# Kernel tuning notes

Measured on AMD Instinct MI355X. Metric: run time of the kernel, lower is better.

Reference implementation:

```python
import jax, jax.numpy as jnp
import numpy as np

EPS = 1e-6
NUM_HEADS = 16

def layer_norm(x, w, b):
    mu = jnp.mean(x, axis=-1, keepdims=True)
    var = jnp.mean(jnp.square(x - mu), axis=-1, keepdims=True)
    return (x - mu) * jax.lax.rsqrt(var + EPS) * w + b

def setup_inputs() -> dict:
    key = jax.random.key(0)
    ks = jax.random.split(key, 8)
    B, N, C = 32, 577, 1024
    H = 4 * C
    s = lambda d: 1.0 / np.sqrt(d)
    return {
        "x": jax.random.normal(ks[0], (B, N, C), jnp.float32),
        "ln1_w": jnp.ones((C,), jnp.float32),
        "ln1_b": jnp.zeros((C,), jnp.float32),
        "qkv_w": jax.random.normal(ks[1], (3 * C, C), jnp.float32) * s(C),
        "qkv_b": jnp.zeros((3 * C,), jnp.float32),
        "proj_w": jax.random.normal(ks[2], (C, C), jnp.float32) * s(C),
        "proj_b": jnp.zeros((C,), jnp.float32),
        "ln2_w": jnp.ones((C,), jnp.float32),
        "ln2_b": jnp.zeros((C,), jnp.float32),
        "fc1_w": jax.random.normal(ks[3], (H, C), jnp.float32) * s(C),
        "fc1_b": jnp.zeros((H,), jnp.float32),
        "fc2_w": jax.random.normal(ks[4], (C, H), jnp.float32) * s(H),
        "fc2_b": jnp.zeros((C,), jnp.float32),
    }

def reference(x, ln1_w, ln1_b, qkv_w, qkv_b, proj_w, proj_b,
              ln2_w, ln2_b, fc1_w, fc1_b, fc2_w, fc2_b):
    B, N, C = x.shape
    Hh = NUM_HEADS
    Dh = C // Hh
    scale = Dh ** -0.5

    # --- attention branch ---
    h = layer_norm(x, ln1_w, ln1_b)
    qkv = h @ qkv_w.T + qkv_b                      # [B,N,3C]
    qkv = qkv.reshape(B, N, 3, Hh, Dh).transpose(2, 0, 3, 1, 4)  # [3,B,H,N,Dh]
    q, k, v = qkv[0] * scale, qkv[1], qkv[2]
    attn = jnp.einsum("bhqd,bhkd->bhqk", q, k)     # [B,H,N,N]
    attn = jax.nn.softmax(attn, axis=-1)
    o = jnp.einsum("bhqk,bhkd->bhqd", attn, v)     # [B,H,N,Dh]
    o = o.transpose(0, 2, 1, 3).reshape(B, N, C)
    x = x + (o @ proj_w.T + proj_b)

    # --- MLP branch ---
    h = layer_norm(x, ln2_w, ln2_b)
    h = jax.nn.gelu(h @ fc1_w.T + fc1_b, approximate=False)
    x = x + (h @ fc2_w.T + fc2_b)
    return x
```

## Files before the change

kernel.cpp:

```cpp
#include <hip/hip_runtime.h>
#include <math.h>

#define BATCH  32
#define NTOK   577
#define CDIM   1024
#define C3DIM  3072
#define H4DIM  4096
#define NHEAD  16
#define MROWS  (BATCH * NTOK)
#define NPADV  584

typedef __bf16 bf16x8 __attribute__((ext_vector_type(8)));
typedef float  f32x4  __attribute__((ext_vector_type(4)));
typedef unsigned short u16x8 __attribute__((ext_vector_type(8)));

__device__ __forceinline__ float bf2f(unsigned short u) {
    union { unsigned int i; float f; } v; v.i = ((unsigned int)u) << 16; return v.f;
}
__device__ __forceinline__ unsigned short f2bf(float f) {
    union { float f; unsigned int i; } v; v.f = f;
    unsigned int r = v.i + 0x7FFFu + ((v.i >> 16) & 1u);
    return (unsigned short)(r >> 16);
}
__device__ __forceinline__ bf16x8 ld_bf8(const unsigned short* p) {
    return __builtin_bit_cast(bf16x8, *(const u16x8*)p);
}

typedef const __attribute__((address_space(1))) unsigned int* gptr_t;
typedef __attribute__((address_space(3))) unsigned int* lptr_t;
__device__ __forceinline__ void gl2lds(const void* g, const void* l) {
    __builtin_amdgcn_global_load_lds(
        (gptr_t)(unsigned long long)g,
        (lptr_t)(unsigned int)(unsigned long long)l,
        16, 0, 0);
}

#define QSCALE 0.18033688011112042f

__global__ __launch_bounds__(256) void conv_kernel(const float* __restrict__ src,
                                                   unsigned short* __restrict__ dst, int n) {
    int i = (blockIdx.x * 256 + threadIdx.x) * 4;
    if (i < n) {
        float4 v = *(const float4*)(src + i);
        dst[i]     = f2bf(v.x);
        dst[i + 1] = f2bf(v.y);
        dst[i + 2] = f2bf(v.z);
        dst[i + 3] = f2bf(v.w);
    }
}

template<bool F32IN>
__global__ __launch_bounds__(256) void ln_kernel(
    const void* __restrict__ X,
    const float* __restrict__ w,
    const float* __restrict__ b,
    unsigned short* __restrict__ out)
{
    const int row = blockIdx.x;
    const int t = threadIdx.x;
    float vals[4]; float s = 0.f, ss = 0.f;
#pragma unroll
    for (int i = 0; i < 4; i++) {
        int c = t + i * 256;
        float v;
        if (F32IN) v = ((const float*)X)[(size_t)row * CDIM + c];
        else       v = bf2f(((const unsigned short*)X)[(size_t)row * CDIM + c]);
        vals[i] = v; s += v; ss += v * v;
    }
#pragma unroll
    for (int off = 32; off > 0; off >>= 1) { s += __shfl_xor(s, off); ss += __shfl_xor(ss, off); }
    __shared__ float red[8];
    if ((t & 63) == 0) { red[t >> 6] = s; red[4 + (t >> 6)] = ss; }
    __syncthreads();
    s  = red[0] + red[1] + red[2] + red[3];
    ss = red[4] + red[5] + red[6] + red[7];
    float mu  = s * (1.f / CDIM);
    float var = ss * (1.f / CDIM) - mu * mu;
    float rs  = rsqrtf(var + 1e-6f);
#pragma unroll
    for (int i = 0; i < 4; i++) {
        int c = t + i * 256;
        float o = (vals[i] - mu) * rs * w[c] + b[c];
        out[(size_t)row * CDIM + c] = f2bf(o);
    }
}

template<int OP>
__global__ __launch_bounds__(512, 2) void gemm256(
    const unsigned short* __restrict__ A,
    const unsigned short* __restrict__ W, int Wstride,
    const unsigned short* __restrict__ bias,
    const void* __restrict__ Res,
    void* __restrict__ Out,
    void* __restrict__ Out2,
    void* __restrict__ Out3,
    int K, int Nout)
{
    __shared__ __align__(16) unsigned short Alds[2][256 * 64];
    __shared__ __align__(16) unsigned short Blds[2][256 * 64];

    const int tid  = threadIdx.x;
    const int lane = tid & 63, wave = tid >> 6;
    const int q = lane >> 4, l16 = lane & 15;
    const int wm = (wave >> 2) << 7;
    const int wn = (wave & 3) << 6;
    const int tileM = blockIdx.y << 8, tileN = blockIdx.x << 8;

    f32x4 acc[8][4];
#pragma unroll
    for (int i = 0; i < 8; i++)
#pragma unroll
        for (int j = 0; j < 4; j++) acc[i][j] = (f32x4){0.f, 0.f, 0.f, 0.f};

    const int srow = tid >> 3;
    const int scol = (tid & 7) << 3;
    const unsigned short* pA[4];
    const unsigned short* pB[4];
#pragma unroll
    for (int j = 0; j < 4; j++) {
        int ra = tileM + j * 64 + srow; if (ra > MROWS - 1) ra = MROWS - 1;
        pA[j] = A + (size_t)ra * K + scol;
        pB[j] = W + (size_t)(tileN + j * 64 + srow) * Wstride + scol;
    }

    auto STAGE = [&](int buf, int k0) {
#pragma unroll
        for (int j = 0; j < 4; j++) {
            gl2lds(pA[j] + k0, &Alds[buf][j * 4096 + wave * 512]);
            gl2lds(pB[j] + k0, &Blds[buf][j * 4096 + wave * 512]);
        }
    };

    auto COMPUTE = [&](int buf) {
#pragma unroll
        for (int ks = 0; ks < 2; ks++) {
            bf16x8 af[8], bfr[4];
#pragma unroll
            for (int mi = 0; mi < 8; mi++)
                af[mi] = ld_bf8(&Alds[buf][(wm + mi * 16 + l16) * 64 + ks * 32 + q * 8]);
#pragma unroll
            for (int ni = 0; ni < 4; ni++)
                bfr[ni] = ld_bf8(&Blds[buf][(wn + ni * 16 + l16) * 64 + ks * 32 + q * 8]);
#pragma unroll
            for (int mi = 0; mi < 8; mi++)
#pragma unroll
                for (int ni = 0; ni < 4; ni++)
                    acc[mi][ni] = __builtin_amdgcn_mfma_f32_16x16x32_bf16(af[mi], bfr[ni], acc[mi][ni], 0, 0, 0);
        }
    };

    const int NT = K >> 6;
    STAGE(0, 0);
    __syncthreads();
    int cur = 0;
    for (int t = 0; t < NT; ++t) {
        if (t + 1 < NT) STAGE(cur ^ 1, (t + 1) << 6);
        COMPUTE(cur);
        __syncthreads();
        cur ^= 1;
    }

#pragma unroll
    for (int mi = 0; mi < 8; mi++) {
#pragma unroll
        for (int r = 0; r < 4; r++) {
            int row = tileM + wm + mi * 16 + q * 4 + r;
            if (row >= MROWS) continue;
            unsigned int bb = 0, nn = 0;
            if constexpr (OP == 0) {
                bb = ((unsigned int)row * 58154u) >> 25;
                nn = (unsigned int)row - bb * 577u;
            }
#pragma unroll
            for (int ni = 0; ni < 4; ni++) {
                int col = tileN + wn + ni * 16 + l16;
                size_t oidx = (size_t)row * Nout + col;
                float v = acc[mi][ni][r];
                if constexpr (OP != 4) v += bf2f(bias[col]);
                if constexpr (OP == 0) {
                    int s = col >> 10, h = (col >> 6) & 15, d = col & 63;
                    size_t bh = (size_t)(bb * 16 + h);
                    if (s == 0)      ((unsigned short*)Out )[(bh * NTOK + nn) * 64 + d] = f2bf(v * QSCALE);
                    else if (s == 1) ((unsigned short*)Out2)[(bh * NTOK + nn) * 64 + d] = f2bf(v);
                    else             ((unsigned short*)Out3)[(bh * 64 + d) * NPADV + nn] = f2bf(v);
                } else if constexpr (OP == 1) {
                    v += ((const float*)Res)[oidx];
                    ((unsigned short*)Out)[oidx] = f2bf(v);
                } else if constexpr (OP == 2) {
                    float z = exp2f(v * fmaf(v * v, 0.1029432f, 2.3022082f));
                    v = v - v * __builtin_amdgcn_rcpf(1.0f + z);
                    ((unsigned short*)Out)[oidx] = f2bf(v);
                } else if constexpr (OP == 3) {
                    v += bf2f(((const unsigned short*)Res)[oidx]);
                    ((float*)Out)[oidx] = v;
                } else {
                    ((float*)Out)[oidx] += v;
                }
            }
        }
    }
}

__global__ __launch_bounds__(256) void attn_kernel(
    const unsigned short* __restrict__ Qb,
    const unsigned short* __restrict__ Kb,
    const unsigned short* __restrict__ Vt,
    unsigned short* __restrict__ o)
{
    const int flat = blockIdx.x;
    const int x8 = flat & 7;
    const int g = flat >> 3;
    const int qt = g % 10;
    const int bh = (g / 10) * 8 + x8;
    const int q0 = qt * 64;
    const int tid = threadIdx.x;
    const int wv = tid >> 6, lane = tid & 63;
    const int qd = lane >> 4, l16 = lane & 15;

    __shared__ __align__(16) unsigned short Ps[4][16 * 72];

    const unsigned short* Qh = Qb + (size_t)bh * NTOK * 64;
    const unsigned short* Kh = Kb + (size_t)bh * NTOK * 64;
    const unsigned short* Vh = Vt + (size_t)bh * 64 * NPADV;

    int qrow = q0 + wv * 16 + l16;
    int qr = qrow < NTOK ? qrow : NTOK - 1;
    bf16x8 qf0 = ld_bf8(Qh + (size_t)qr * 64 + qd * 8);
    bf16x8 qf1 = ld_bf8(Qh + (size_t)qr * 64 + 32 + qd * 8);

    float lsum[4];
    f32x4 Oacc[4];
#pragma unroll
    for (int r = 0; r < 4; r++) lsum[r] = 0.f;
#pragma unroll
    for (int ni = 0; ni < 4; ni++) Oacc[ni] = (f32x4){0.f, 0.f, 0.f, 0.f};

    for (int kt = 0; kt < 10; kt++) {
        const int k0 = kt * 64;
        const bool tail = (kt == 9);
        f32x4 sacc[4];
#pragma unroll
        for (int ni = 0; ni < 4; ni++) sacc[ni] = (f32x4){0.f, 0.f, 0.f, 0.f};
#pragma unroll
        for (int ni = 0; ni < 4; ni++) {
            int krow = k0 + ni * 16 + l16;
            if (krow > NTOK - 1) krow = NTOK - 1;
            const unsigned short* kp = Kh + (size_t)krow * 64 + qd * 8;
            bf16x8 b0 = ld_bf8(kp);
            bf16x8 b1 = ld_bf8(kp + 32);
            sacc[ni] = __builtin_amdgcn_mfma_f32_16x16x32_bf16(qf0, b0, sacc[ni], 0, 0, 0);
            sacc[ni] = __builtin_amdgcn_mfma_f32_16x16x32_bf16(qf1, b1, sacc[ni], 0, 0, 0);
        }

#pragma unroll
        for (int r = 0; r < 4; r++) {
#pragma unroll
            for (int ni = 0; ni < 4; ni++) {
                float pv = exp2f(sacc[ni][r]);
                if (tail && (k0 + ni * 16 + l16 >= NTOK)) pv = 0.f;
                lsum[r] += pv;
                Ps[wv][(qd * 4 + r) * 72 + ni * 16 + l16] = f2bf(pv);
            }
        }

#pragma unroll
        for (int kk = 0; kk < 2; kk++) {
            bf16x8 a = ld_bf8(&Ps[wv][l16 * 72 + kk * 32 + qd * 8]);
            int kchunk = k0 + kk * 32 + qd * 8;
            if (kchunk > NTOK - 1) kchunk = NTOK - 1;
#pragma unroll
            for (int ni = 0; ni < 4; ni++) {
                bf16x8 bb = ld_bf8(Vh + (size_t)(ni * 16 + l16) * NPADV + kchunk);
                Oacc[ni] = __builtin_amdgcn_mfma_f32_16x16x32_bf16(a, bb, Oacc[ni], 0, 0, 0);
            }
        }
    }

#pragma unroll
    for (int r = 0; r < 4; r++)
#pragma unroll
        for (int off = 8; off > 0; off >>= 1) lsum[r] += __shfl_xor(lsum[r], off);

    const int b = bh >> 4, h = bh & 15;
#pragma unroll
    for (int r = 0; r < 4; r++) {
        int gq = q0 + wv * 16 + qd * 4 + r;
        if (gq >= NTOK) continue;
        float inv = 1.0f / lsum[r];
#pragma unroll
        for (int ni = 0; ni < 4; ni++) {
            int d = ni * 16 + l16;
            o[((size_t)b * NTOK + gq) * CDIM + (size_t)h * 64 + d] = f2bf(Oacc[ni][r] * inv);
        }
    }
}

extern "C" void kernel_launch(void* const* d_in, const int* in_sizes, int n_in,
                              void* d_out, int out_size, void* d_ws, size_t ws_size,
                              hipStream_t stream) {
    (void)in_sizes; (void)n_in; (void)out_size;
    const float* x      = (const float*)d_in[0];
    const float* ln1_w  = (const float*)d_in[1];
    const float* ln1_b  = (const float*)d_in[2];
    const float* qkv_w  = (const float*)d_in[3];
    const float* qkv_b  = (const float*)d_in[4];
    const float* proj_w = (const float*)d_in[5];
    const float* proj_b = (const float*)d_in[6];
    const float* ln2_w  = (const float*)d_in[7];
    const float* ln2_b  = (const float*)d_in[8];
    const float* fc1_w  = (const float*)d_in[9];
    const float* fc1_b  = (const float*)d_in[10];
    const float* fc2_w  = (const float*)d_in[11];
    const float* fc2_b  = (const float*)d_in[12];

    char* ws = (char*)d_ws;
    size_t off = 0;
    auto alloc = [&](size_t els) { void* p = ws + off; off += els * 2; return (unsigned short*)p; };
    unsigned short* qkvw_b  = alloc(3145728);
    unsigned short* projw_b = alloc(1048576);
    unsigned short* fc1w_b  = alloc(4194304);
    unsigned short* fc2w_b  = alloc(4194304);
    unsigned short* qkvb_b  = alloc(3072);
    unsigned short* projb_b = alloc(1024);
    unsigned short* fc1b_b  = alloc(4096);
    unsigned short* fc2b_b  = alloc(1024);
    off = (off + 255) & ~(size_t)255;
    unsigned short* R1 = (unsigned short*)(ws + off); off += (size_t)MROWS * 1024 * 2;
    unsigned short* R2 = (unsigned short*)(ws + off); off += (size_t)512 * 64 * NPADV * 2;
    unsigned short* R3 = (unsigned short*)(ws + off);
    size_t rem = ws_size > off ? ws_size - off : 0;
    const int CH = rem >= (size_t)MROWS * H4DIM * 2 ? H4DIM
                 : (rem >= (size_t)MROWS * 1024 * 2 ? 1024
                 : (rem >= (size_t)MROWS * 512 * 2 ? 512 : 256));

    unsigned short* Qb   = (unsigned short*)d_out;
    unsigned short* h1   = Qb + (size_t)MROWS * 1024;
    unsigned short* obuf = h1;
    unsigned short* Kb = R1;
    unsigned short* Vt = R2;
    unsigned short* x1 = R1;
    unsigned short* h2 = R2;

    conv_kernel<<<3145728 / 1024, 256, 0, stream>>>(qkv_w,  qkvw_b,  3145728);
    conv_kernel<<<1048576 / 1024, 256, 0, stream>>>(proj_w, projw_b, 1048576);
    conv_kernel<<<4194304 / 1024, 256, 0, stream>>>(fc1_w,  fc1w_b,  4194304);
    conv_kernel<<<4194304 / 1024, 256, 0, stream>>>(fc2_w,  fc2w_b,  4194304);
    conv_kernel<<<3, 256, 0, stream>>>(qkv_b,  qkvb_b,  3072);
    conv_kernel<<<1, 256, 0, stream>>>(proj_b, projb_b, 1024);
    conv_kernel<<<4, 256, 0, stream>>>(fc1_b,  fc1b_b,  4096);
    conv_kernel<<<1, 256, 0, stream>>>(fc2_b,  fc2b_b,  1024);

    const int mt = (MROWS + 255) / 256;

    ln_kernel<true><<<MROWS, 256, 0, stream>>>(x, ln1_w, ln1_b, h1);
    gemm256<0><<<dim3(C3DIM / 256, mt), 512, 0, stream>>>(
        h1, qkvw_b, CDIM, qkvb_b, nullptr, Qb, Kb, Vt, CDIM, C3DIM);
    attn_kernel<<<5120, 256, 0, stream>>>(Qb, Kb, Vt, obuf);
    gemm256<1><<<dim3(CDIM / 256, mt), 512, 0, stream>>>(
        obuf, projw_b, CDIM, projb_b, x, x1, nullptr, nullptr, CDIM, CDIM);
    ln_kernel<false><<<MROWS, 256, 0, stream>>>(x1, ln2_w, ln2_b, h2);

    if (CH == H4DIM) {
        gemm256<2><<<dim3(H4DIM / 256, mt), 512, 0, stream>>>(
            h2, fc1w_b, CDIM, fc1b_b, nullptr, R3, nullptr, nullptr, CDIM, H4DIM);
        gemm256<3><<<dim3(CDIM / 256, mt), 512, 0, stream>>>(
            R3, fc2w_b, H4DIM, fc2b_b, x1, d_out, nullptr, nullptr, H4DIM, CDIM);
    } else {
        for (int c0 = 0; c0 < H4DIM; c0 += CH) {
            gemm256<2><<<dim3(CH / 256, mt), 512, 0, stream>>>(
                h2, fc1w_b + (size_t)c0 * CDIM, CDIM, fc1b_b + c0, nullptr, R3, nullptr, nullptr, CDIM, CH);
            if (c0 == 0)
                gemm256<3><<<dim3(CDIM / 256, mt), 512, 0, stream>>>(
                    R3, fc2w_b, H4DIM, fc2b_b, x1, d_out, nullptr, nullptr, CH, CDIM);
            else
                gemm256<4><<<dim3(CDIM / 256, mt), 512, 0, stream>>>(
                    R3, fc2w_b + c0, H4DIM, nullptr, nullptr, d_out, nullptr, nullptr, CH, CDIM);
        }
    }
}
```

Baseline: 1.263 ms.

## Use 128x128 tile GEMM for N=1024 projection and fc2 layers

Adds a smaller 128x128-tile GEMM kernel with 256 threads and uses it for the attention projection and fc2 GEMMs, whose output width of 1024 gave few blocks with 256x256 tiles. The large-tile kernel is kept only for the QKV and fc1 GEMMs, and its epilogue is simplified accordingly. The goal is better CU occupancy and load balance on the narrow GEMMs. The cost is less data reuse and a single-buffered, sync-heavy K loop in the new kernel.

```diff
diff --git a/kernel.cpp b/kernel.cpp
--- a/kernel.cpp
+++ b/kernel.cpp
@@ -36,6 +36,11 @@
 }
 
 #define QSCALE 0.18033688011112042f
+
+__device__ __forceinline__ float gelu_f(float v) {
+    float z = exp2f(v * fmaf(v * v, 0.1029432f, 2.3022082f));
+    return v - v * __builtin_amdgcn_rcpf(1.0f + z);
+}
 
 __global__ __launch_bounds__(256) void conv_kernel(const float* __restrict__ src,
                                                    unsigned short* __restrict__ dst, int n) {
@@ -86,11 +91,87 @@
 }
 
 template<int OP>
+__global__ __launch_bounds__(256) void gemm128(
+    const unsigned short* __restrict__ A,
+    const unsigned short* __restrict__ W, int Wstride,
+    const unsigned short* __restrict__ bias,
+    const void* __restrict__ Res,
+    void* __restrict__ Out,
+    int K, int Nout)
+{
+    __shared__ __align__(16) unsigned short Alds[128 * 32];
+    __shared__ __align__(16) unsigned short Blds[128 * 32];
+    const int tid  = threadIdx.x;
+    const int lane = tid & 63, wave = tid >> 6;
+    const int q = lane >> 4, l16 = lane & 15;
+    const int wm = (wave & 1) << 6, wn = (wave >> 1) << 6;
+    const int tileM = blockIdx.y << 7, tileN = blockIdx.x << 7;
+
+    f32x4 acc[4][4];
+#pragma unroll
+    for (int i = 0; i < 4; i++)
+#pragma unroll
+        for (int j = 0; j < 4; j++) acc[i][j] = (f32x4){0.f, 0.f, 0.f, 0.f};
+
+    const int srow = tid >> 2;
+    const int soff = (tid & 3) << 3;
+    int arow1 = tileM + srow;       if (arow1 > MROWS - 1) arow1 = MROWS - 1;
+    int arow2 = tileM + srow + 64;  if (arow2 > MROWS - 1) arow2 = MROWS - 1;
+    const unsigned short* Aptr  = A + (size_t)arow1 * K + soff;
+    const unsigned short* Aptr2 = A + (size_t)arow2 * K + soff;
+    const unsigned short* Wp    = W + (size_t)(tileN + srow) * Wstride + soff;
+    const unsigned short* Wp2   = Wp + (size_t)64 * Wstride;
+
+    for (int k0 = 0; k0 < K; k0 += 32) {
+        __syncthreads();
+        gl2lds(Aptr  + k0, &Alds[wave * 512]);
+        gl2lds(Aptr2 + k0, &Alds[2048 + wave * 512]);
+        gl2lds(Wp    + k0, &Blds[wave * 512]);
+        gl2lds(Wp2   + k0, &Blds[2048 + wave * 512]);
+        __syncthreads();
+        bf16x8 af[4], bfr[4];
+#pragma unroll
+        for (int mi = 0; mi < 4; mi++) af[mi]  = ld_bf8(&Alds[(wm + mi * 16 + l16) * 32 + q * 8]);
+#pragma unroll
+        for (int ni = 0; ni < 4; ni++) bfr[ni] = ld_bf8(&Blds[(wn + ni * 16 + l16) * 32 + q * 8]);
+#pragma unroll
+        for (int mi = 0; mi < 4; mi++)
+#pragma unroll
+            for (int ni = 0; ni < 4; ni++)
+                acc[mi][ni] = __builtin_amdgcn_mfma_f32_16x16x32_bf16(af[mi], bfr[ni], acc[mi][ni], 0, 0, 0);
+    }
+
+#pragma unroll
+    for (int mi = 0; mi < 4; mi++) {
+#pragma unroll
+        for (int r = 0; r < 4; r++) {
+            int row = tileM + wm + mi * 16 + q * 4 + r;
+            if (row >= MROWS) continue;
+#pragma unroll
+            for (int ni = 0; ni < 4; ni++) {
+                int col = tileN + wn + ni * 16 + l16;
+                size_t oidx = (size_t)row * Nout + col;
+                float v = acc[mi][ni][r];
+                if constexpr (OP != 4) v += bf2f(bias[col]);
+                if constexpr (OP == 1) {
+                    v += ((const float*)Res)[oidx];
+                    ((unsigned short*)Out)[oidx] = f2bf(v);
+                } else if constexpr (OP == 3) {
+                    v += bf2f(((const unsigned short*)Res)[oidx]);
+                    ((float*)Out)[oidx] = v;
+                } else {
+                    ((float*)Out)[oidx] += v;
+                }
+            }
+        }
+    }
+}
+
+template<int OP>
 __global__ __launch_bounds__(512, 2) void gemm256(
     const unsigned short* __restrict__ A,
     const unsigned short* __restrict__ W, int Wstride,
     const unsigned short* __restrict__ bias,
-    const void* __restrict__ Res,
     void* __restrict__ Out,
     void* __restrict__ Out2,
     void* __restrict__ Out3,
@@ -175,26 +256,15 @@
             for (int ni = 0; ni < 4; ni++) {
                 int col = tileN + wn + ni * 16 + l16;
                 size_t oidx = (size_t)row * Nout + col;
-                float v = acc[mi][ni][r];
-                if constexpr (OP != 4) v += bf2f(bias[col]);
+                float v = acc[mi][ni][r] + bf2f(bias[col]);
                 if constexpr (OP == 0) {
                     int s = col >> 10, h = (col >> 6) & 15, d = col & 63;
                     size_t bh = (size_t)(bb * 16 + h);
                     if (s == 0)      ((unsigned short*)Out )[(bh * NTOK + nn) * 64 + d] = f2bf(v * QSCALE);
                     else if (s == 1) ((unsigned short*)Out2)[(bh * NTOK + nn) * 64 + d] = f2bf(v);
                     else             ((unsigned short*)Out3)[(bh * 64 + d) * NPADV + nn] = f2bf(v);
-                } else if constexpr (OP == 1) {
-                    v += ((const float*)Res)[oidx];
-                    ((unsigned short*)Out)[oidx] = f2bf(v);
-                } else if constexpr (OP == 2) {
-                    float z = exp2f(v * fmaf(v * v, 0.1029432f, 2.3022082f));
-                    v = v - v * __builtin_amdgcn_rcpf(1.0f + z);
-                    ((unsigned short*)Out)[oidx] = f2bf(v);
-                } else if constexpr (OP == 3) {
-                    v += bf2f(((const unsigned short*)Res)[oidx]);
-                    ((float*)Out)[oidx] = v;
                 } else {
-                    ((float*)Out)[oidx] += v;
+                    ((unsigned short*)Out)[oidx] = f2bf(gelu_f(v));
                 }
             }
         }
@@ -350,31 +420,32 @@
     conv_kernel<<<4, 256, 0, stream>>>(fc1_b,  fc1b_b,  4096);
     conv_kernel<<<1, 256, 0, stream>>>(fc2_b,  fc2b_b,  1024);
 
-    const int mt = (MROWS + 255) / 256;
+    const int mt128 = (MROWS + 127) / 128;
+    const int mt256 = (MROWS + 255) / 256;
 
     ln_kernel<true><<<MROWS, 256, 0, stream>>>(x, ln1_w, ln1_b, h1);
-    gemm256<0><<<dim3(C3DIM / 256, mt), 512, 0, stream>>>(
-        h1, qkvw_b, CDIM, qkvb_b, nullptr, Qb, Kb, Vt, CDIM, C3DIM);
+    gemm256<0><<<dim3(C3DIM / 256, mt256), 512, 0, stream>>>(
+        h1, qkvw_b, CDIM, qkvb_b, Qb, Kb, Vt, CDIM, C3DIM);
     attn_kernel<<<5120, 256, 0, stream>>>(Qb, Kb, Vt, obuf);
-    gemm256<1><<<dim3(CDIM / 256, mt), 512, 0, stream>>>(
-        obuf, projw_b, CDIM, projb_b, x, x1, nullptr, nullptr, CDIM, CDIM);
+    gemm128<1><<<dim3(CDIM / 128, mt128), 256, 0, stream>>>(
+        obuf, projw_b, CDIM, projb_b, x, x1, CDIM, CDIM);
     ln_kernel<false><<<MROWS, 256, 0, stream>>>(x1, ln2_w, ln2_b, h2);
 
     if (CH == H4DIM) {
-        gemm256<2><<<dim3(H4DIM / 256, mt), 512, 0, stream>>>(
-            h2, fc1w_b, CDIM, fc1b_b, nullptr, R3, nullptr, nullptr, CDIM, H4DIM);
-        gemm256<3><<<dim3(CDIM / 256, mt), 512, 0, stream>>>(
-            R3, fc2w_b, H4DIM, fc2b_b, x1, d_out, nullptr, nullptr, H4DIM, CDIM);
+        gemm256<2><<<dim3(H4DIM / 256, mt256), 512, 0, stream>>>(
+            h2, fc1w_b, CDIM, fc1b_b, R3, nullptr, nullptr, CDIM, H4DIM);
+        gemm128<3><<<dim3(CDIM / 128, mt128), 256, 0, stream>>>(
+            R3, fc2w_b, H4DIM, fc2b_b, x1, d_out, H4DIM, CDIM);
     } else {
         for (int c0 = 0; c0 < H4DIM; c0 += CH) {
-            gemm256<2><<<dim3(CH / 256, mt), 512, 0, stream>>>(
-                h2, fc1w_b + (size_t)c0 * CDIM, CDIM, fc1b_b + c0, nullptr, R3, nullptr, nullptr, CDIM, CH);
+            gemm256<2><<<dim3(CH / 256, mt256), 512, 0, stream>>>(
+                h2, fc1w_b + (size_t)c0 * CDIM, CDIM, fc1b_b + c0, R3, nullptr, nullptr, CDIM, CH);
             if (c0 == 0)
-                gemm256<3><<<dim3(CDIM / 256, mt), 512, 0, stream>>>(
-                    R3, fc2w_b, H4DIM, fc2b_b, x1, d_out, nullptr, nullptr, CH, CDIM);
+                gemm128<3><<<dim3(CDIM / 128, mt128), 256, 0, stream>>>(
+                    R3, fc2w_b, H4DIM, fc2b_b, x1, d_out, CH, CDIM);
             else
-                gemm256<4><<<dim3(CDIM / 256, mt), 512, 0, stream>>>(
-                    R3, fc2w_b + c0, H4DIM, nullptr, nullptr, d_out, nullptr, nullptr, CH, CDIM);
-        }
-    }
-}
+                gemm128<4><<<dim3(CDIM / 128, mt128), 256, 0, stream>>>(
+                    R3, fc2w_b + c0, H4DIM, nullptr, nullptr, d_out, CH, CDIM);
+        }
+    }
+}
```

Result: faster. 1.230 ms (-2.7%).
